# Optimization experiments

Hardware: AMD Instinct MI355X
Metric: run time of the kernel (lower is better)

Reference implementation:

```python
import jax, jax.numpy as jnp
import numpy as np

B, S, IN, H = 16, 512, 512, 256
TAU_TRACE = 20.0
TAU_MEM = 20.0
DECAY_TRACE = float(np.exp(-1.0 / TAU_TRACE))  # exp_convolve decay
DECAY_MEM = float(np.exp(-1.0 / TAU_MEM))      # leaky-integrator dynamics decay
LR = 0.01                                       # plasticity learning rate
W_MAX = 1.0                                     # soft upper bound on fast weights


def setup_inputs() -> dict:
    key = jax.random.key(0)
    k1, k2 = jax.random.split(key)
    x = jax.random.normal(k1, (B, S, IN), dtype=jnp.float32)
    # xavier_uniform with gain=sqrt(2) on W of shape [2H, IN]
    lim = float(np.sqrt(2.0) * np.sqrt(6.0 / (2 * H + IN)))
    W = jax.random.uniform(k2, (2 * H, IN), dtype=jnp.float32, minval=-lim, maxval=lim)
    return {"x": x, "W": W}


def reference(x, W):
    # i = x @ W^T : [B, S, 2H], then split into key/value input currents
    i = jnp.einsum('bsi,hi->bsh', x, W)
    ik, iv = jnp.split(i, 2, axis=2)  # each [B, S, H]
    bsz = x.shape[0]
    h = W.shape[0] // 2

    def step(carry, inp):
        kv, vv, kt, vt, mem = carry
        ik_t, iv_t = inp  # [B, H] each
        # key dynamics (leaky integrator + tanh)
        kv = DECAY_MEM * kv + ik_t
        key = jnp.tanh(kv)
        # memory readout: 0.2 * (key.unsqueeze(1) * mem).sum(2) == 0.2 * mem @ key
        ikv = 0.2 * jnp.einsum('bij,bj->bi', mem, key)
        # value dynamics
        vv = DECAY_MEM * vv + iv_t + ikv
        val = jnp.tanh(vv)
        # exponential traces
        kt = DECAY_TRACE * kt + (1.0 - DECAY_TRACE) * key
        vt = DECAY_TRACE * vt + (1.0 - DECAY_TRACE) * val
        # soft-bounded Hebbian outer-product fast-weight update
        mem = mem + LR * (vt[:, :, None] * kt[:, None, :]) * (W_MAX - mem)
        return (kv, vv, kt, vt, mem), (key, val)

    z = jnp.zeros((bsz, h), x.dtype)
    mem0 = jnp.zeros((bsz, h, h), x.dtype)
    (_, _, _, _, mem), (keys, vals) = jax.lax.scan(
        step, (z, z, z, z, mem0),
        (jnp.swapaxes(ik, 0, 1), jnp.swapaxes(iv, 0, 1)))  # scan over time
    return mem, jnp.swapaxes(keys, 0, 1), jnp.swapaxes(vals, 0, 1)
```

## Files before the change

### kernel.cpp

```cpp
#include <hip/hip_runtime.h>

#define BB 16
#define SS 512
#define KIN 512
#define H 256

typedef float v2f __attribute__((ext_vector_type(2)));

constexpr float DECAY = 0.951229424500714f;
constexpr float OMD   = 0.048770575499286f;
constexpr float LR    = 0.01f;

__device__ __forceinline__ float fast_tanh(float x) {
    float e = __expf(2.f * x);
    return 1.f - __fdividef(2.f, e + 1.f);
}

__device__ __forceinline__ v2f pk_mul(v2f a, v2f b) {
    v2f d; asm("v_pk_mul_f32 %0, %1, %2" : "=v"(d) : "v"(a), "v"(b)); return d;
}
__device__ __forceinline__ v2f pk_fma(v2f a, v2f b, v2f c) {
    v2f d; asm("v_pk_fma_f32 %0, %1, %2, %3" : "=v"(d) : "v"(a), "v"(b), "v"(c)); return d;
}

__device__ __forceinline__ float allred32(float x) {
    int t;
    t = __builtin_amdgcn_update_dpp(0, __float_as_int(x), 0x111, 0xf, 0xf, false);
    x += __int_as_float(t);
    t = __builtin_amdgcn_update_dpp(0, __float_as_int(x), 0x112, 0xf, 0xf, false);
    x += __int_as_float(t);
    t = __builtin_amdgcn_update_dpp(0, __float_as_int(x), 0x114, 0xf, 0xf, false);
    x += __int_as_float(t);
    t = __builtin_amdgcn_update_dpp(0, __float_as_int(x), 0x118, 0xf, 0xf, false);
    x += __int_as_float(t);
    t = __builtin_amdgcn_update_dpp(0, __float_as_int(x), 0x142, 0xa, 0xf, false);
    x += __int_as_float(t);
    return __int_as_float(__builtin_amdgcn_ds_swizzle(__float_as_int(x), 0x3E0));
}

__global__ __launch_bounds__(256) void gemm_xwT(const float* __restrict__ X,
                                                const float* __restrict__ W,
                                                float* __restrict__ ik_out,
                                                float* __restrict__ iv_t) {
    __shared__ float As[16][68];
    __shared__ float Bs[16][68];
    const int m0 = blockIdx.y * 64;
    const int n0 = blockIdx.x * 64;
    const int tid = threadIdx.x;
    const int r  = tid >> 2;
    const int cg = tid & 3;
    const int tx = tid & 15;
    const int ty = tid >> 4;
    float acc[4][4] = {};
    for (int k0 = 0; k0 < KIN; k0 += 16) {
        float4 av = *(const float4*)&X[(size_t)(m0 + r) * KIN + k0 + cg * 4];
        float4 bv = *(const float4*)&W[(size_t)(n0 + r) * KIN + k0 + cg * 4];
        __syncthreads();
        As[cg*4+0][r] = av.x; As[cg*4+1][r] = av.y; As[cg*4+2][r] = av.z; As[cg*4+3][r] = av.w;
        Bs[cg*4+0][r] = bv.x; Bs[cg*4+1][r] = bv.y; Bs[cg*4+2][r] = bv.z; Bs[cg*4+3][r] = bv.w;
        __syncthreads();
#pragma unroll
        for (int kk = 0; kk < 16; ++kk) {
            float4 a = *(const float4*)&As[kk][ty * 4];
            float4 b = *(const float4*)&Bs[kk][tx * 4];
            float ar[4] = {a.x, a.y, a.z, a.w};
            float br[4] = {b.x, b.y, b.z, b.w};
#pragma unroll
            for (int i = 0; i < 4; ++i)
#pragma unroll
                for (int j = 0; j < 4; ++j) acc[i][j] += ar[i] * br[j];
        }
    }
    if (n0 < 256) {
#pragma unroll
        for (int i = 0; i < 4; ++i) {
            float4 o = make_float4(acc[i][0], acc[i][1], acc[i][2], acc[i][3]);
            *(float4*)&ik_out[(size_t)(m0 + ty * 4 + i) * 256 + n0 + tx * 4] = o;
        }
    } else {
        const int b  = m0 >> 9;
        const int s0 = (m0 & 511) + ty * 4;
#pragma unroll
        for (int j = 0; j < 4; ++j) {
            float4 o = make_float4(acc[0][j], acc[1][j], acc[2][j], acc[3][j]);
            *(float4*)&iv_t[((size_t)b * H + (n0 - 256 + tx * 4 + j)) * SS + s0] = o;
        }
    }
}

__global__ __launch_bounds__(64) void key_scan(const float* __restrict__ ik,
                                               float* __restrict__ keys) {
    const int idx = blockIdx.x * 64 + threadIdx.x;
    const int b   = idx >> 8;
    const int col = idx & 255;
    const float* c  = ik + (size_t)b * SS * 256 + col;
    float* ko = keys + (size_t)b * SS * H + col;
    float kv = 0.f;
    constexpr int D = 32;
    float ib[D];
#pragma unroll
    for (int j = 0; j < D; ++j) ib[j] = c[(size_t)j * 256];
    for (int t = 0; t < SS; t += D) {
#pragma unroll
        for (int j = 0; j < D; ++j) {
            float v = ib[j];
            int tn = t + D + j; if (tn > SS - 1) tn = SS - 1;
            ib[j] = c[(size_t)tn * 256];
            kv = DECAY * kv + v;
            ko[(size_t)(t + j) * H] = fast_tanh(kv);
        }
    }
}

__global__ __launch_bounds__(256, 2) void value_scan(const float* __restrict__ keys,
                                                     const float* __restrict__ iv_t,
                                                     float* __restrict__ mem_out,
                                                     float* __restrict__ vals) {
    const int tid  = threadIdx.x;
    const int wave = tid >> 6;
    const int lane = tid & 63;
    const int sub  = lane & 31;
    const int half = lane >> 5;
    const int b    = blockIdx.x & 15;
    const int rg   = blockIdx.x >> 4;
    const int row  = rg * 8 + wave * 2 + half;
    const int so   = sub * 8;

    const float* kp  = keys + (size_t)b * SS * H + so;
    const float* ivp = iv_t + ((size_t)b * H + row) * SS;
    float* vrow = vals + (size_t)b * SS * H + row;

    const v2f DEC2 = {DECAY, DECAY};
    const v2f OMD2 = {OMD, OMD};

    v2f nm0 = {0.f,0.f}, nm1 = {0.f,0.f}, nm2 = {0.f,0.f}, nm3 = {0.f,0.f};
    v2f w0  = {0.f,0.f}, w1  = {0.f,0.f}, w2  = {0.f,0.f}, w3  = {0.f,0.f};
    v2f kt0 = {0.f,0.f}, kt1 = {0.f,0.f}, kt2 = {0.f,0.f}, kt3 = {0.f,0.f};
    float vv = 0.f, vt = 0.f, c = 0.f, ar = 0.f, br = 0.f, stash = 0.f;

    v2f kp0 = *(const v2f*)(kp + 0), kp1 = *(const v2f*)(kp + 2),
        kp2 = *(const v2f*)(kp + 4), kp3 = *(const v2f*)(kp + 6);
    v2f kR[4][4];
#pragma unroll
    for (int j = 0; j < 4; ++j)
#pragma unroll
        for (int q = 0; q < 4; ++q)
            kR[j][q] = *(const v2f*)(kp + (size_t)(1 + j) * H + q * 2);
    const float* kpF = kp + 5 * H;

    float4 iA0 = *(const float4*)(ivp + 0);
    float4 iA1 = *(const float4*)(ivp + 4);
    float4 iB0 = *(const float4*)(ivp + 8);
    float4 iB1 = *(const float4*)(ivp + 12);
    ivp += 16;

#define VS_STEP(J, RELK)                                                       \
    {                                                                          \
        v2f kc0 = kR[(J)&3][0], kc1 = kR[(J)&3][1],                            \
            kc2 = kR[(J)&3][2], kc3 = kR[(J)&3][3];                            \
        if (RELK) {                                                            \
            kR[(J)&3][0] = *(const v2f*)(kpF + ((J)&3) * H + 0);               \
            kR[(J)&3][1] = *(const v2f*)(kpF + ((J)&3) * H + 2);               \
            kR[(J)&3][2] = *(const v2f*)(kpF + ((J)&3) * H + 4);               \
            kR[(J)&3][3] = *(const v2f*)(kpF + ((J)&3) * H + 6);               \
        }                                                                      \
                                        \
        v2f nc2 = {-c, -c};                                                    \
        nm0 = pk_fma(nc2, w0, nm0);                                            \
        nm1 = pk_fma(nc2, w1, nm1);                                            \
        nm2 = pk_fma(nc2, w2, nm2);                                            \
        nm3 = pk_fma(nc2, w3, nm3);                       \
        kt0 = pk_fma(DEC2, kt0, pk_mul(OMD2, kp0));                            \
        kt1 = pk_fma(DEC2, kt1, pk_mul(OMD2, kp1));                            \
        kt2 = pk_fma(DEC2, kt2, pk_mul(OMD2, kp2));                            \
        kt3 = pk_fma(DEC2, kt3, pk_mul(OMD2, kp3));      \
        w0 = pk_fma(kt0, nm0, kt0);                                            \
        w1 = pk_fma(kt1, nm1, kt1);                                            \
        w2 = pk_fma(kt2, nm2, kt2);                                            \
        w3 = pk_fma(kt3, nm3, kt3);               \
        v2f a2 = pk_mul(nm0, kc0);                                             \
        a2 = pk_fma(nm1, kc1, a2);                                             \
        a2 = pk_fma(nm2, kc2, a2);                                             \
        a2 = pk_fma(nm3, kc3, a2);                     \
        v2f b2 = pk_mul(w0, kc0);                                              \
        b2 = pk_fma(w1, kc1, b2);                                              \
        b2 = pk_fma(w2, kc2, b2);                                              \
        b2 = pk_fma(w3, kc3, b2);                       \
        float arn = -0.2f * allred32(a2.x + a2.y);                             \
        float brn =  0.2f * allred32(b2.x + b2.y);                             \
        kp0 = kc0; kp1 = kc1; kp2 = kc2; kp3 = kc3;       \
                                                          \
        float vvt = __builtin_fmaf(DECAY, vv, ivs[J]) + ar;                    \
        vv = __builtin_fmaf(c, br, vvt);                                       \
        float valv = fast_tanh(vv);                                            \
        vt = __builtin_fmaf(DECAY, vt, OMD * valv);                            \
        if (sub == (J)) stash = valv;                                          \
        c = LR * vt;                                                           \
        ar = arn; br = brn;                                                    \
        asm volatile("" ::: "memory");                                         \
    }

    for (int t0 = 0; t0 < SS - 16; t0 += 16) {
        float4 nA0 = *(const float4*)(ivp + 0);
        float4 nA1 = *(const float4*)(ivp + 4);
        float4 nB0 = *(const float4*)(ivp + 8);
        float4 nB1 = *(const float4*)(ivp + 12);
        ivp += 16;
        {
            float ivs[16] = {iA0.x, iA0.y, iA0.z, iA0.w,
                             iA1.x, iA1.y, iA1.z, iA1.w,
                             iB0.x, iB0.y, iB0.z, iB0.w,
                             iB1.x, iB1.y, iB1.z, iB1.w};
            VS_STEP(0, 1)  VS_STEP(1, 1)  VS_STEP(2, 1)  VS_STEP(3, 1)
            kpF += 4 * H;
            VS_STEP(4, 1)  VS_STEP(5, 1)  VS_STEP(6, 1)  VS_STEP(7, 1)
            kpF += 4 * H;
            VS_STEP(8, 1)  VS_STEP(9, 1)  VS_STEP(10, 1) VS_STEP(11, 1)
            kpF += 4 * H;
            VS_STEP(12, 1) VS_STEP(13, 1) VS_STEP(14, 1) VS_STEP(15, 1)
            kpF += 4 * H;
        }
        if (sub < 16) vrow[(size_t)sub * H] = stash;
        vrow += 16 * H;
        iA0 = nA0; iA1 = nA1; iB0 = nB0; iB1 = nB1;
    }
    {
        float ivs[16] = {iA0.x, iA0.y, iA0.z, iA0.w,
                         iA1.x, iA1.y, iA1.z, iA1.w,
                         iB0.x, iB0.y, iB0.z, iB0.w,
                         iB1.x, iB1.y, iB1.z, iB1.w};
        VS_STEP(0, 1)  VS_STEP(1, 1)  VS_STEP(2, 1)  VS_STEP(3, 1)
        kpF += 4 * H;
        VS_STEP(4, 1)  VS_STEP(5, 1)  VS_STEP(6, 1)  VS_STEP(7, 1)
        kpF += 4 * H;
        VS_STEP(8, 1)  VS_STEP(9, 1)  VS_STEP(10, 1) VS_STEP(11, 0)
        VS_STEP(12, 0) VS_STEP(13, 0) VS_STEP(14, 0) VS_STEP(15, 0)
        if (sub < 16) vrow[(size_t)sub * H] = stash;
    }
#undef VS_STEP

    {
        v2f ncf = {-c, -c};
        nm0 = pk_fma(ncf, w0, nm0);
        nm1 = pk_fma(ncf, w1, nm1);
        nm2 = pk_fma(ncf, w2, nm2);
        nm3 = pk_fma(ncf, w3, nm3);
    }
    float* mo = &mem_out[((size_t)b * H + row) * H + so];
    *(float4*)&mo[0] = make_float4(-nm0.x, -nm0.y, -nm1.x, -nm1.y);
    *(float4*)&mo[4] = make_float4(-nm2.x, -nm2.y, -nm3.x, -nm3.y);
}

extern "C" void kernel_launch(void* const* d_in, const int* in_sizes, int n_in,
                              void* d_out, int out_size, void* d_ws, size_t ws_size,
                              hipStream_t stream) {
    const float* x = (const float*)d_in[0];
    const float* W = (const float*)d_in[1];
    float* out = (float*)d_out;
    float* mem_out = out;
    float* keys = out + (size_t)BB * H * H;
    float* vals = keys + (size_t)BB * SS * H;
    float* ik   = (float*)d_ws;
    float* iv_t = ik + (size_t)BB * SS * 256;

    dim3 gb(8, 128);
    gemm_xwT<<<gb, 256, 0, stream>>>(x, W, ik, iv_t);
    key_scan<<<64, 64, 0, stream>>>(ik, keys);
    value_scan<<<512, 256, 0, stream>>>(keys, iv_t, mem_out, vals);
}
```

Baseline: 264.1 us.

## Parallelize key scan with chunked three-pass linear recurrence

Replaces the sequential 512-step key leaky-integrator scan, which ran on only 64 blocks of 64 threads, with a chunked parallel scan. The first pass computes per-chunk partial sums over 8 chunks of 64 steps, the second propagates carries using decay^64, and the third re-scans each chunk from its carry and emits tanh keys. This raises parallelism 8x for a latency-bound recurrence. In exchange it reads ik twice, adds two kernel launches, and uses the vals output buffer as scratch before value_scan overwrites it.

```diff
diff --git a/kernel.cpp b/kernel.cpp
--- a/kernel.cpp
+++ b/kernel.cpp
@@ -7,9 +7,10 @@
 
 typedef float v2f __attribute__((ext_vector_type(2)));
 
-constexpr float DECAY = 0.951229424500714f;
-constexpr float OMD   = 0.048770575499286f;
-constexpr float LR    = 0.01f;
+constexpr float DECAY   = 0.951229424500714f;
+constexpr float OMD     = 0.048770575499286f;
+constexpr float DECAY64 = 0.040762203978366f;
+constexpr float LR      = 0.01f;
 
 __device__ __forceinline__ float fast_tanh(float x) {
     float e = __expf(2.f * x);
@@ -88,26 +89,66 @@
     }
 }
 
-__global__ __launch_bounds__(64) void key_scan(const float* __restrict__ ik,
-                                               float* __restrict__ keys) {
+
+__global__ __launch_bounds__(256) void ks1_chunk(const float* __restrict__ ik,
+                                                 float* __restrict__ E) {
+    const int tid  = blockIdx.x * 256 + threadIdx.x;
+    const int col  = tid & 255;
+    const int rest = tid >> 8;
+    const int b    = rest >> 3;
+    const int ch   = rest & 7;
+    const float* p = ik + ((size_t)(b * SS + ch * 64)) * 256 + col;
+    float e = 0.f;
+    float rb[4];
+#pragma unroll
+    for (int j = 0; j < 4; ++j) rb[j] = p[(size_t)j * 256];
+    for (int j0 = 0; j0 < 64; j0 += 4) {
+#pragma unroll
+        for (int j = 0; j < 4; ++j) {
+            float v = rb[j];
+            int jn = j0 + 4 + j; if (jn > 63) jn = 63;
+            rb[j] = p[(size_t)jn * 256];
+            e = __builtin_fmaf(DECAY, e, v);
+        }
+    }
+    E[((size_t)b * 8 + ch) * 256 + col] = e;
+}
+
+__global__ __launch_bounds__(64) void ks2_carry(const float* __restrict__ E,
+                                                float* __restrict__ Sst) {
     const int idx = blockIdx.x * 64 + threadIdx.x;
     const int b   = idx >> 8;
     const int col = idx & 255;
-    const float* c  = ik + (size_t)b * SS * 256 + col;
-    float* ko = keys + (size_t)b * SS * H + col;
-    float kv = 0.f;
-    constexpr int D = 32;
-    float ib[D];
-#pragma unroll
-    for (int j = 0; j < D; ++j) ib[j] = c[(size_t)j * 256];
-    for (int t = 0; t < SS; t += D) {
-#pragma unroll
-        for (int j = 0; j < D; ++j) {
-            float v = ib[j];
-            int tn = t + D + j; if (tn > SS - 1) tn = SS - 1;
-            ib[j] = c[(size_t)tn * 256];
-            kv = DECAY * kv + v;
-            ko[(size_t)(t + j) * H] = fast_tanh(kv);
+    float carry = 0.f;
+#pragma unroll
+    for (int c = 0; c < 8; ++c) {
+        Sst[((size_t)b * 8 + c) * 256 + col] = carry;
+        carry = __builtin_fmaf(DECAY64, carry, E[((size_t)b * 8 + c) * 256 + col]);
+    }
+}
+
+__global__ __launch_bounds__(256) void ks3_emit(const float* __restrict__ ik,
+                                                const float* __restrict__ Sst,
+                                                float* __restrict__ keys) {
+    const int tid  = blockIdx.x * 256 + threadIdx.x;
+    const int col  = tid & 255;
+    const int rest = tid >> 8;
+    const int b    = rest >> 3;
+    const int ch   = rest & 7;
+    const float* p = ik + ((size_t)(b * SS + ch * 64)) * 256 + col;
+    float* ko = keys + ((size_t)(b * SS + ch * 64)) * H + col;
+    float kv = Sst[((size_t)b * 8 + ch) * 256 + col];
+    float rb[4];
+#pragma unroll
+    for (int j = 0; j < 4; ++j) rb[j] = p[(size_t)j * 256];
+    for (int j0 = 0; j0 < 64; j0 += 4) {
+#pragma unroll
+        for (int j = 0; j < 4; ++j) {
+            float v = rb[j];
+            int jn = j0 + 4 + j; if (jn > 63) jn = 63;
+            rb[j] = p[(size_t)jn * 256];
+            kv = __builtin_fmaf(DECAY, kv, v);
+            ko[(size_t)(j0 + j) * H] = fast_tanh(kv);
         }
     }
 }
@@ -164,32 +205,30 @@
             kR[(J)&3][2] = *(const v2f*)(kpF + ((J)&3) * H + 4);               \
             kR[(J)&3][3] = *(const v2f*)(kpF + ((J)&3) * H + 6);               \
         }                                                                      \
-                                        \
         v2f nc2 = {-c, -c};                                                    \
         nm0 = pk_fma(nc2, w0, nm0);                                            \
         nm1 = pk_fma(nc2, w1, nm1);                                            \
         nm2 = pk_fma(nc2, w2, nm2);                                            \
-        nm3 = pk_fma(nc2, w3, nm3);                       \
+        nm3 = pk_fma(nc2, w3, nm3);                                            \
         kt0 = pk_fma(DEC2, kt0, pk_mul(OMD2, kp0));                            \
         kt1 = pk_fma(DEC2, kt1, pk_mul(OMD2, kp1));                            \
         kt2 = pk_fma(DEC2, kt2, pk_mul(OMD2, kp2));                            \
-        kt3 = pk_fma(DEC2, kt3, pk_mul(OMD2, kp3));      \
+        kt3 = pk_fma(DEC2, kt3, pk_mul(OMD2, kp3));                            \
         w0 = pk_fma(kt0, nm0, kt0);                                            \
         w1 = pk_fma(kt1, nm1, kt1);                                            \
         w2 = pk_fma(kt2, nm2, kt2);                                            \
-        w3 = pk_fma(kt3, nm3, kt3);               \
+        w3 = pk_fma(kt3, nm3, kt3);                                            \
         v2f a2 = pk_mul(nm0, kc0);                                             \
         a2 = pk_fma(nm1, kc1, a2);                                             \
         a2 = pk_fma(nm2, kc2, a2);                                             \
-        a2 = pk_fma(nm3, kc3, a2);                     \
+        a2 = pk_fma(nm3, kc3, a2);                                             \
         v2f b2 = pk_mul(w0, kc0);                                              \
         b2 = pk_fma(w1, kc1, b2);                                              \
         b2 = pk_fma(w2, kc2, b2);                                              \
-        b2 = pk_fma(w3, kc3, b2);                       \
+        b2 = pk_fma(w3, kc3, b2);                                              \
         float arn = -0.2f * allred32(a2.x + a2.y);                             \
         float brn =  0.2f * allred32(b2.x + b2.y);                             \
-        kp0 = kc0; kp1 = kc1; kp2 = kc2; kp3 = kc3;       \
-                                                          \
+        kp0 = kc0; kp1 = kc1; kp2 = kc2; kp3 = kc3;                            \
         float vvt = __builtin_fmaf(DECAY, vv, ivs[J]) + ar;                    \
         vv = __builtin_fmaf(c, br, vvt);                                       \
         float valv = fast_tanh(vv);                                            \
@@ -262,9 +301,13 @@
     float* vals = keys + (size_t)BB * SS * H;
     float* ik   = (float*)d_ws;
     float* iv_t = ik + (size_t)BB * SS * 256;
+    float* E    = vals;
+    float* Sst  = vals + 32768;
 
     dim3 gb(8, 128);
     gemm_xwT<<<gb, 256, 0, stream>>>(x, W, ik, iv_t);
-    key_scan<<<64, 64, 0, stream>>>(ik, keys);
+    ks1_chunk<<<128, 256, 0, stream>>>(ik, E);
+    ks2_carry<<<64, 64, 0, stream>>>(E, Sst);
+    ks3_emit<<<128, 256, 0, stream>>>(ik, Sst, keys);
     value_scan<<<512, 256, 0, stream>>>(keys, iv_t, mem_out, vals);
 }
```

Result: faster. 243.5 us (-7.8%).
